# Kernel tuning notes

Measured on AMD Instinct MI355X. Metric: run time of the kernel, lower is better.

## Reference

```python
import jax, jax.numpy as jnp
import numpy as np

D = 768

def _linear_params(key, name_idx, d_in, d_out):
    k1, k2 = jax.random.split(jax.random.fold_in(jax.random.key(42), name_idx))
    bound = 1.0 / np.sqrt(d_in)
    W = jax.random.uniform(k1, (d_out, d_in), jnp.float32, -bound, bound)
    b = jax.random.uniform(k2, (d_out,), jnp.float32, -bound, bound)
    return W, b

def setup_inputs() -> dict:
    key = jax.random.key(0)
    kq, kk, kv = jax.random.split(key, 3)
    B, S = 8, 2048
    inp = {
        'query': jax.random.normal(kq, (B, S, D), jnp.float32),
        'key': jax.random.normal(kk, (B, S, D), jnp.float32),
        'value': jax.random.normal(kv, (B, S, D), jnp.float32),
    }
    Wq, bq = _linear_params(key, 0, D, D)
    Wk, bk = _linear_params(key, 1, D, D)
    Wv, bv = _linear_params(key, 2, D, D)
    Wg1, bg1 = _linear_params(key, 3, D, D)
    Wg2, bg2 = _linear_params(key, 4, D, D)
    inp.update(Wq=Wq, bq=bq, Wk=Wk, bk=bk, Wv=Wv, bv=bv,
               Wg1=Wg1, bg1=bg1, Wg2=Wg2, bg2=bg2,
               text_scale=jnp.ones((1, D), jnp.float32))
    return inp

def reference(query, key, value, Wq, bq, Wk, bk, Wv, bv, Wg1, bg1, Wg2, bg2, text_scale):
    # Linear projections (torch Linear: x @ W.T + b)
    q = jnp.einsum('bsd,ed->bse', query, Wq) + bq
    k = jnp.einsum('bsd,ed->bse', key, Wk) + bk
    v = jnp.einsum('bsd,ed->bse', value, Wv) + bv
    scale = 1.0 / jnp.sqrt(jnp.float32(k.shape[-1]))
    scores = jnp.einsum('bqd,bkd->bqk', q, k) * scale  # [B, S, S]
    attn = jax.nn.softmax(scores, axis=-1)
    attended = jnp.einsum('bqk,bkd->bqd', attn, v)  # dropout = identity (eval)
    # text_gate: Linear -> ReLU -> Linear -> Sigmoid, then sigmoid applied AGAIN (faithful)
    h = jax.nn.relu(jnp.einsum('bsd,ed->bse', attended, Wg1) + bg1)
    gate = jax.nn.sigmoid(jnp.einsum('bsd,ed->bse', h, Wg2) + bg2)
    gated = jax.nn.sigmoid(gate) * attended * text_scale
    return gated
```

## Files before the change

### kernel.cpp

```cpp
#include <hip/hip_runtime.h>

typedef unsigned short ushort_t;
typedef __bf16 bf16x8 __attribute__((ext_vector_type(8)));
typedef float f32x4 __attribute__((ext_vector_type(4)));
typedef short short8 __attribute__((ext_vector_type(8)));

__device__ __forceinline__ float bf2f(unsigned short u) {
    union { unsigned int i; float f; } v; v.i = ((unsigned int)u) << 16; return v.f;
}
__device__ __forceinline__ unsigned short f2bf(float f) {
    union { float f; unsigned int i; } v; v.f = f;
    unsigned int r = v.i + 0x7fffu + ((v.i >> 16) & 1u);
    return (unsigned short)(r >> 16);
}
__device__ __forceinline__ float sigm(float x) { return 1.0f / (1.0f + __expf(-x)); }

__device__ __forceinline__ void async_copy16(const ushort_t* src, ushort_t* dst_lds) {
    __builtin_amdgcn_global_load_lds(
        (const __attribute__((address_space(1))) void*)src,
        (__attribute__((address_space(3))) void*)dst_lds,
        16, 0, 0);
}

#define WSEG 589824
#define NWALL 2949120
#define NTOT 2953728
__global__ __launch_bounds__(256)
void convert_params(const float* __restrict__ Wq, const float* __restrict__ Wk,
                    const float* __restrict__ Wv, const float* __restrict__ Wg1,
                    const float* __restrict__ Wg2, const float* __restrict__ bq,
                    const float* __restrict__ bk, const float* __restrict__ bv,
                    const float* __restrict__ bg1, const float* __restrict__ bg2,
                    const float* __restrict__ ts, ushort_t* __restrict__ dst)
{
    int i = (blockIdx.x * 256 + threadIdx.x) * 8;
    if (i >= NTOT) return;
    const float* src; int off;
    if (i < NWALL) {
        int wi = i / WSEG; off = i - wi * WSEG;
        src = (wi == 0) ? Wq : (wi == 1) ? Wk : (wi == 2) ? Wv : (wi == 3) ? Wg1 : Wg2;
    } else {
        int j = i - NWALL; int bi = j / 768; off = j - bi * 768;
        src = (bi == 0) ? bq : (bi == 1) ? bk : (bi == 2) ? bv : (bi == 3) ? bg1 : (bi == 4) ? bg2 : ts;
    }
    float4 a = *(const float4*)(src + off);
    float4 b = *(const float4*)(src + off + 4);
    short8 o;
    o[0] = (short)f2bf(a.x); o[1] = (short)f2bf(a.y); o[2] = (short)f2bf(a.z); o[3] = (short)f2bf(a.w);
    o[4] = (short)f2bf(b.x); o[5] = (short)f2bf(b.y); o[6] = (short)f2bf(b.z); o[7] = (short)f2bf(b.w);
    *(short8*)(dst + i) = o;
}

template<int EPI, int AF32, int CF32>
__global__ __launch_bounds__(256, 2)
void gemm_bt(const void* __restrict__ Av, const ushort_t* __restrict__ B,
             void* __restrict__ Cv, const ushort_t* __restrict__ bias,
             const ushort_t* __restrict__ aux, const ushort_t* __restrict__ ts,
             int M, int N, int K, float scale,
             long long batchA, long long batchB, long long batchC)
{
    __shared__ __align__(16) ushort_t As[128 * 32];
    __shared__ __align__(16) ushort_t Bs[128 * 32];
    const int tid  = threadIdx.x;
    const int lane = tid & 63;
    const int wave = tid >> 6;
    const int wr = wave >> 1, wc = wave & 1;

    const int gx = gridDim.x, gy = gridDim.y;
    const int nwg = gx * gy * gridDim.z;
    int fid = (blockIdx.z * gy + blockIdx.y) * gx + blockIdx.x;
    fid = (fid & 7) * (nwg >> 3) + (fid >> 3);
    const int bz  = fid / (gx * gy);
    const int rem = fid - bz * (gx * gy);
    const int by  = rem / gx;
    const int bx  = rem - by * gx;
    const int row0 = by * 128;
    const int col0 = bx * 128;

    f32x4 acc[4][4] = {};

    const int srow = tid >> 2;
    const int scol = (tid & 3) * 8;
    const ushort_t* ga0 = (const ushort_t*)Av + batchA * bz + (size_t)(row0 + srow) * K + scol;
    const ushort_t* gb0 = B + batchB * bz + (size_t)(col0 + srow) * K + scol;
    const int arow_s = tid >> 1;
    const int acol_s = (tid & 1) * 16;
    const float* gaf = (const float*)Av + batchA * bz + (size_t)(row0 + arow_s) * K + acol_s;

    const int kop  = (lane >> 4) * 8;
    const int arow = wr * 64 + (lane & 15);
    const int brow = wc * 64 + (lane & 15);

    for (int k0 = 0; k0 < K; k0 += 32) {
        if (AF32) {
            float4 fa0 = *(const float4*)(gaf + k0);
            float4 fa1 = *(const float4*)(gaf + k0 + 4);
            float4 fa2 = *(const float4*)(gaf + k0 + 8);
            float4 fa3 = *(const float4*)(gaf + k0 + 12);
            async_copy16(gb0 + k0,                  Bs + tid * 8);
            async_copy16(gb0 + (size_t)64 * K + k0, Bs + 2048 + tid * 8);
            short8 p0, p1;
            p0[0] = (short)f2bf(fa0.x); p0[1] = (short)f2bf(fa0.y);
            p0[2] = (short)f2bf(fa0.z); p0[3] = (short)f2bf(fa0.w);
            p0[4] = (short)f2bf(fa1.x); p0[5] = (short)f2bf(fa1.y);
            p0[6] = (short)f2bf(fa1.z); p0[7] = (short)f2bf(fa1.w);
            p1[0] = (short)f2bf(fa2.x); p1[1] = (short)f2bf(fa2.y);
            p1[2] = (short)f2bf(fa2.z); p1[3] = (short)f2bf(fa2.w);
            p1[4] = (short)f2bf(fa3.x); p1[5] = (short)f2bf(fa3.y);
            p1[6] = (short)f2bf(fa3.z); p1[7] = (short)f2bf(fa3.w);
            *(short8*)(As + arow_s * 32 + acol_s)     = p0;
            *(short8*)(As + arow_s * 32 + acol_s + 8) = p1;
        } else {
            async_copy16(ga0 + k0,                  As + tid * 8);
            async_copy16(ga0 + (size_t)64 * K + k0, As + 2048 + tid * 8);
            async_copy16(gb0 + k0,                  Bs + tid * 8);
            async_copy16(gb0 + (size_t)64 * K + k0, Bs + 2048 + tid * 8);
        }
        asm volatile("s_waitcnt vmcnt(0)" ::: "memory");
        __syncthreads();

        bf16x8 af[4], bfr[4];
        #pragma unroll
        for (int m = 0; m < 4; ++m)
            af[m] = *(const bf16x8*)(As + (arow + m * 16) * 32 + kop);
        #pragma unroll
        for (int n = 0; n < 4; ++n)
            bfr[n] = *(const bf16x8*)(Bs + (brow + n * 16) * 32 + kop);
        #pragma unroll
        for (int m = 0; m < 4; ++m)
            #pragma unroll
            for (int n = 0; n < 4; ++n)
                acc[m][n] = __builtin_amdgcn_mfma_f32_16x16x32_bf16(af[m], bfr[n], acc[m][n], 0, 0, 0);
        __syncthreads();
    }

    const int r0 = row0 + wr * 64 + (lane >> 4) * 4;
    const int c0 = col0 + wc * 64 + (lane & 15);
    #pragma unroll
    for (int m = 0; m < 4; ++m) {
        #pragma unroll
        for (int n = 0; n < 4; ++n) {
            const int col = c0 + n * 16;
            #pragma unroll
            for (int r = 0; r < 4; ++r) {
                const int row = r0 + m * 16 + r;
                float val = acc[m][n][r];
                if (EPI == 1) {
                    val += bf2f(bias[col]);
                } else if (EPI == 2) {
                    val *= scale;
                } else if (EPI == 3) {
                    val += bf2f(bias[col]);
                    val = fmaxf(val, 0.0f);
                } else if (EPI == 4) {
                    val += bf2f(bias[col]);
                    float g  = sigm(val);
                    float gg = sigm(g);
                    val = gg * bf2f(aux[(size_t)row * N + col]) * bf2f(ts[col]);
                }
                if (CF32) ((float*)Cv)[batchC * bz + (size_t)row * N + col] = val;
                else      ((ushort_t*)Cv)[batchC * bz + (size_t)row * N + col] = f2bf(val);
            }
        }
    }
}

__global__ __launch_bounds__(256)
void softmax_inplace(ushort_t* __restrict__ P, int S)
{
    const size_t row = blockIdx.x;
    ushort_t* p = P + row * (size_t)S;
    const int tid = threadIdx.x;
    const int lane = tid & 63, wave = tid >> 6;

    short8 raw = *(const short8*)(p + tid * 8);
    float x[8];
    #pragma unroll
    for (int j = 0; j < 8; ++j) x[j] = bf2f((unsigned short)raw[j]);

    float mx = x[0];
    #pragma unroll
    for (int j = 1; j < 8; ++j) mx = fmaxf(mx, x[j]);
    #pragma unroll
    for (int o = 32; o > 0; o >>= 1) mx = fmaxf(mx, __shfl_xor(mx, o));
    __shared__ float redm[4], reds[4];
    if (lane == 0) redm[wave] = mx;
    __syncthreads();
    mx = fmaxf(fmaxf(redm[0], redm[1]), fmaxf(redm[2], redm[3]));

    float s = 0.f;
    #pragma unroll
    for (int j = 0; j < 8; ++j) { x[j] = __expf(x[j] - mx); s += x[j]; }
    #pragma unroll
    for (int o = 32; o > 0; o >>= 1) s += __shfl_xor(s, o);
    if (lane == 0) reds[wave] = s;
    __syncthreads();
    s = reds[0] + reds[1] + reds[2] + reds[3];
    const float inv = 1.0f / s;

    short8 outv;
    #pragma unroll
    for (int j = 0; j < 8; ++j) outv[j] = (short)f2bf(x[j] * inv);
    *(short8*)(p + tid * 8) = outv;
}

__global__ __launch_bounds__(256)
void transpose2d(const ushort_t* __restrict__ V, ushort_t* __restrict__ VT, int R, int Ccols)
{
    __shared__ ushort_t t[32][33];
    const size_t zoff = (size_t)blockIdx.z * R * Ccols;
    const int tx = threadIdx.x, ty = threadIdx.y;
    const int c = blockIdx.x * 32 + tx;
    const int rbase = blockIdx.y * 32;
    #pragma unroll
    for (int i = 0; i < 4; ++i)
        t[ty + i * 8][tx] = V[zoff + (size_t)(rbase + ty + i * 8) * Ccols + c];
    __syncthreads();
    const int r = rbase + tx;
    const int cbase = blockIdx.x * 32;
    #pragma unroll
    for (int i = 0; i < 4; ++i)
        VT[zoff + (size_t)(cbase + ty + i * 8) * R + r] = t[tx][ty + i * 8];
}

extern "C" void kernel_launch(void* const* d_in, const int* in_sizes, int n_in,
                              void* d_out, int out_size, void* d_ws, size_t ws_size,
                              hipStream_t stream)
{
    (void)in_sizes; (void)n_in; (void)out_size;
    const float* query = (const float*)d_in[0];
    const float* key_  = (const float*)d_in[1];
    const float* value = (const float*)d_in[2];
    const float* Wq  = (const float*)d_in[3];
    const float* bq  = (const float*)d_in[4];
    const float* Wk  = (const float*)d_in[5];
    const float* bk  = (const float*)d_in[6];
    const float* Wv  = (const float*)d_in[7];
    const float* bv  = (const float*)d_in[8];
    const float* Wg1 = (const float*)d_in[9];
    const float* bg1 = (const float*)d_in[10];
    const float* Wg2 = (const float*)d_in[11];
    const float* bg2 = (const float*)d_in[12];
    const float* tsc = (const float*)d_in[13];

    const int S = 2048, D = 768, Bc = 8;
    const int MS = Bc * S;
    const long long SD = (long long)S * D;
    const long long SS = (long long)S * S;

    char* ws = (char*)d_ws;
    ushort_t* q   = (ushort_t*)(ws);
    ushort_t* att = q;
    ushort_t* k   = (ushort_t*)(ws + 25165824ll);
    ushort_t* h   = k;
    ushort_t* vT  = (ushort_t*)(ws + 50331648ll);
    ushort_t* Wb  = (ushort_t*)(ws + 75497472ll);
    ushort_t* P   = (ushort_t*)(ws + 81404928ll);
    ushort_t* v   = (ushort_t*)d_out;

    const int WQ = 0, WK = 589824, WV = 1179648, WG1 = 1769472, WG2 = 2359296;
    const int BQ = 2949120, BK = 2949888, BV = 2950656, BG1 = 2951424, BG2 = 2952192, TSO = 2952960;

    const dim3 blk(256);
    const float scale = 0.03608439182435161f;
    const bool batched = ws_size >= 148513792ull;

    convert_params<<<dim3((NTOT / 8 + 255) / 256), blk, 0, stream>>>(
        Wq, Wk, Wv, Wg1, Wg2, bq, bk, bv, bg1, bg2, tsc, Wb);
    gemm_bt<1, 1, 0><<<dim3(D / 128, MS / 128), blk, 0, stream>>>(query, Wb + WQ, q, Wb + BQ, nullptr, nullptr, MS, D, D, 1.f, 0, 0, 0);
    gemm_bt<1, 1, 0><<<dim3(D / 128, MS / 128), blk, 0, stream>>>(key_,  Wb + WK, k, Wb + BK, nullptr, nullptr, MS, D, D, 1.f, 0, 0, 0);
    gemm_bt<1, 1, 0><<<dim3(D / 128, MS / 128), blk, 0, stream>>>(value, Wb + WV, v, Wb + BV, nullptr, nullptr, MS, D, D, 1.f, 0, 0, 0);
    transpose2d<<<dim3(D / 32, S / 32, Bc), dim3(32, 8), 0, stream>>>(v, vT, S, D);
    if (batched) {
        gemm_bt<2, 0, 0><<<dim3(S / 128, S / 128, Bc), blk, 0, stream>>>(q, k, P, nullptr, nullptr, nullptr, S, S, D, scale, SD, SD, SS);
        softmax_inplace<<<dim3(MS), blk, 0, stream>>>(P, S);
        gemm_bt<0, 0, 0><<<dim3(D / 128, S / 128, Bc), blk, 0, stream>>>(P, vT, att, nullptr, nullptr, nullptr, S, D, S, 1.f, SS, SD, SD);
    } else {
        for (int z = 0; z < Bc; ++z) {
            gemm_bt<2, 0, 0><<<dim3(S / 128, S / 128), blk, 0, stream>>>(q + (size_t)z * SD, k + (size_t)z * SD, P,
                                                                          nullptr, nullptr, nullptr, S, S, D, scale, 0, 0, 0);
            softmax_inplace<<<dim3(S), blk, 0, stream>>>(P, S);
            gemm_bt<0, 0, 0><<<dim3(D / 128, S / 128), blk, 0, stream>>>(P, vT + (size_t)z * SD, att + (size_t)z * SD,
                                                                          nullptr, nullptr, nullptr, S, D, S, 1.f, 0, 0, 0);
        }
    }
    gemm_bt<3, 0, 0><<<dim3(D / 128, MS / 128), blk, 0, stream>>>(att, Wb + WG1, h, Wb + BG1, nullptr, nullptr, MS, D, D, 1.f, 0, 0, 0);
    gemm_bt<4, 0, 1><<<dim3(D / 128, MS / 128), blk, 0, stream>>>(h, Wb + WG2, d_out, Wb + BG2, att, Wb + TSO, MS, D, D, 1.f, 0, 0, 0);
}
```

Baseline: 374.7 us.

## Replace 128-tile GEMMs with pipelined 256x256 swizzled-LDS GEMM and batch QKV projections

Replaces the simple single-buffered 128x128 GEMM with a 512-thread 256x256-tile kernel. The new kernel double-buffers 64-wide K chunks in XOR-swizzled LDS, interleaves async global-to-LDS copies with MFMA groups under explicit barriers, and raises priority around MFMAs. The fp32 inputs are pre-converted to bf16 in a separate pass so the three QKV projections run as one z-batched launch. The non-batched fallback path is dropped, and the code now always assumes a large workspace. This trades an extra conversion pass and more LDS and registers for higher data reuse and compute/load overlap.

Result: slower. 385.8 us (+3.0%).

```diff
diff --git a/kernel.cpp b/kernel.cpp
--- a/kernel.cpp
+++ b/kernel.cpp
@@ -4,6 +4,9 @@
 typedef __bf16 bf16x8 __attribute__((ext_vector_type(8)));
 typedef float f32x4 __attribute__((ext_vector_type(4)));
 typedef short short8 __attribute__((ext_vector_type(8)));
+
+#define SBAR()   __builtin_amdgcn_s_barrier()
+#define WAITV4() asm volatile("s_waitcnt vmcnt(4)" ::: "memory")
 
 __device__ __forceinline__ float bf2f(unsigned short u) {
     union { unsigned int i; float f; } v; v.i = ((unsigned int)u) << 16; return v.f;
@@ -20,6 +23,10 @@
         (const __attribute__((address_space(1))) void*)src,
         (__attribute__((address_space(3))) void*)dst_lds,
         16, 0, 0);
+}
+
+__device__ __forceinline__ f32x4 MFMA(bf16x8 a, bf16x8 b, f32x4 c) {
+    return __builtin_amdgcn_mfma_f32_16x16x32_bf16(a, b, c, 0, 0, 0);
 }
 
 #define WSEG 589824
@@ -51,20 +58,77 @@
     *(short8*)(dst + i) = o;
 }
 
-template<int EPI, int AF32, int CF32>
-__global__ __launch_bounds__(256, 2)
-void gemm_bt(const void* __restrict__ Av, const ushort_t* __restrict__ B,
-             void* __restrict__ Cv, const ushort_t* __restrict__ bias,
+#define PERT 12582912ll
+__global__ __launch_bounds__(256)
+void convert_inputs(const float* __restrict__ q, const float* __restrict__ k,
+                    const float* __restrict__ v, ushort_t* __restrict__ X)
+{
+    long long i = ((long long)blockIdx.x * 256 + threadIdx.x) * 8;
+    const float* src; long long off;
+    if (i < PERT)          { src = q; off = i; }
+    else if (i < 2 * PERT) { src = k; off = i - PERT; }
+    else                   { src = v; off = i - 2 * PERT; }
+    float4 a = *(const float4*)(src + off);
+    float4 b = *(const float4*)(src + off + 4);
+    short8 o;
+    o[0] = (short)f2bf(a.x); o[1] = (short)f2bf(a.y); o[2] = (short)f2bf(a.z); o[3] = (short)f2bf(a.w);
+    o[4] = (short)f2bf(b.x); o[5] = (short)f2bf(b.y); o[6] = (short)f2bf(b.z); o[7] = (short)f2bf(b.w);
+    *(short8*)(X + i) = o;
+}
+
+template<int NOFF>
+__device__ __forceinline__ void load_b2(bf16x8 (&bF)[4][2], const ushort_t* Bh, int rbase,
+                                        int l15, int k4, int l7)
+{
+    #pragma unroll
+    for (int n = 0; n < 2; ++n) {
+        const int row = rbase + (NOFF + n) * 16 + l15;
+        bF[NOFF + n][0] = *(const bf16x8*)(Bh + (row << 6) + (((0 + k4) ^ l7) << 3));
+        bF[NOFF + n][1] = *(const bf16x8*)(Bh + (row << 6) + (((4 + k4) ^ l7) << 3));
+    }
+}
+__device__ __forceinline__ void load_a4(bf16x8 (&aF)[4][2], const ushort_t* Ah, int moff,
+                                        int l15, int k4, int l7)
+{
+    #pragma unroll
+    for (int m = 0; m < 4; ++m) {
+        const int row = (moff + m) * 16 + l15;
+        aF[m][0] = *(const bf16x8*)(Ah + (row << 6) + (((0 + k4) ^ l7) << 3));
+        aF[m][1] = *(const bf16x8*)(Ah + (row << 6) + (((4 + k4) ^ l7) << 3));
+    }
+}
+template<int MB, int NB>
+__device__ __forceinline__ void mfma16(f32x4 (&acc)[8][4], const bf16x8 (&aF)[4][2],
+                                       const bf16x8 (&bF)[4][2])
+{
+    __builtin_amdgcn_s_setprio(1);
+    #pragma unroll
+    for (int m = 0; m < 4; ++m)
+        #pragma unroll
+        for (int n = 0; n < 2; ++n) {
+            acc[MB + m][NB + n] = MFMA(aF[m][0], bF[NB + n][0], acc[MB + m][NB + n]);
+            acc[MB + m][NB + n] = MFMA(aF[m][1], bF[NB + n][1], acc[MB + m][NB + n]);
+        }
+    __builtin_amdgcn_s_setprio(0);
+}
+
+template<int EPI, int CF32>
+__global__ __launch_bounds__(512, 1)
+void gemm256(const ushort_t* __restrict__ A, const ushort_t* __restrict__ B,
+             void* __restrict__ Cv, void* __restrict__ Cv2,
+             const ushort_t* __restrict__ bias,
              const ushort_t* __restrict__ aux, const ushort_t* __restrict__ ts,
              int M, int N, int K, float scale,
              long long batchA, long long batchB, long long batchC)
 {
-    __shared__ __align__(16) ushort_t As[128 * 32];
-    __shared__ __align__(16) ushort_t Bs[128 * 32];
+    __shared__ __align__(16) ushort_t As[2][2][8192];
+    __shared__ __align__(16) ushort_t Bs[2][2][8192];
     const int tid  = threadIdx.x;
     const int lane = tid & 63;
-    const int wave = tid >> 6;
-    const int wr = wave >> 1, wc = wave & 1;
+    const int wid  = tid >> 6;
+    const int wr = wid >> 2;
+    const int wc = wid & 3;
+    const int l15 = lane & 15, k4 = lane >> 4, l7 = lane & 7;
 
     const int gx = gridDim.x, gy = gridDim.y;
     const int nwg = gx * gy * gridDim.z;
@@ -74,70 +138,104 @@
     const int rem = fid - bz * (gx * gy);
     const int by  = rem / gx;
     const int bx  = rem - by * gx;
-    const int row0 = by * 128;
-    const int col0 = bx * 128;
-
-    f32x4 acc[4][4] = {};
-
-    const int srow = tid >> 2;
-    const int scol = (tid & 3) * 8;
-    const ushort_t* ga0 = (const ushort_t*)Av + batchA * bz + (size_t)(row0 + srow) * K + scol;
-    const ushort_t* gb0 = B + batchB * bz + (size_t)(col0 + srow) * K + scol;
-    const int arow_s = tid >> 1;
-    const int acol_s = (tid & 1) * 16;
-    const float* gaf = (const float*)Av + batchA * bz + (size_t)(row0 + arow_s) * K + acol_s;
-
-    const int kop  = (lane >> 4) * 8;
-    const int arow = wr * 64 + (lane & 15);
-    const int brow = wc * 64 + (lane & 15);
-
-    for (int k0 = 0; k0 < K; k0 += 32) {
-        if (AF32) {
-            float4 fa0 = *(const float4*)(gaf + k0);
-            float4 fa1 = *(const float4*)(gaf + k0 + 4);
-            float4 fa2 = *(const float4*)(gaf + k0 + 8);
-            float4 fa3 = *(const float4*)(gaf + k0 + 12);
-            async_copy16(gb0 + k0,                  Bs + tid * 8);
-            async_copy16(gb0 + (size_t)64 * K + k0, Bs + 2048 + tid * 8);
-            short8 p0, p1;
-            p0[0] = (short)f2bf(fa0.x); p0[1] = (short)f2bf(fa0.y);
-            p0[2] = (short)f2bf(fa0.z); p0[3] = (short)f2bf(fa0.w);
-            p0[4] = (short)f2bf(fa1.x); p0[5] = (short)f2bf(fa1.y);
-            p0[6] = (short)f2bf(fa1.z); p0[7] = (short)f2bf(fa1.w);
-            p1[0] = (short)f2bf(fa2.x); p1[1] = (short)f2bf(fa2.y);
-            p1[2] = (short)f2bf(fa2.z); p1[3] = (short)f2bf(fa2.w);
-            p1[4] = (short)f2bf(fa3.x); p1[5] = (short)f2bf(fa3.y);
-            p1[6] = (short)f2bf(fa3.z); p1[7] = (short)f2bf(fa3.w);
-            *(short8*)(As + arow_s * 32 + acol_s)     = p0;
-            *(short8*)(As + arow_s * 32 + acol_s + 8) = p1;
-        } else {
-            async_copy16(ga0 + k0,                  As + tid * 8);
-            async_copy16(ga0 + (size_t)64 * K + k0, As + 2048 + tid * 8);
-            async_copy16(gb0 + k0,                  Bs + tid * 8);
-            async_copy16(gb0 + (size_t)64 * K + k0, Bs + 2048 + tid * 8);
-        }
-        asm volatile("s_waitcnt vmcnt(0)" ::: "memory");
-        __syncthreads();
-
-        bf16x8 af[4], bfr[4];
-        #pragma unroll
-        for (int m = 0; m < 4; ++m)
-            af[m] = *(const bf16x8*)(As + (arow + m * 16) * 32 + kop);
-        #pragma unroll
-        for (int n = 0; n < 4; ++n)
-            bfr[n] = *(const bf16x8*)(Bs + (brow + n * 16) * 32 + kop);
-        #pragma unroll
-        for (int m = 0; m < 4; ++m)
-            #pragma unroll
-            for (int n = 0; n < 4; ++n)
-                acc[m][n] = __builtin_amdgcn_mfma_f32_16x16x32_bf16(af[m], bfr[n], acc[m][n], 0, 0, 0);
-        __syncthreads();
-    }
-
-    const int r0 = row0 + wr * 64 + (lane >> 4) * 4;
-    const int c0 = col0 + wc * 64 + (lane & 15);
-    #pragma unroll
-    for (int m = 0; m < 4; ++m) {
+    const int row0 = by * 256;
+    const int col0 = bx * 256;
+
+    const ushort_t* Ab = A + batchA * bz;
+    const ushort_t* Bb = B + batchB * bz;
+
+    const int srow  = tid >> 3;
+    const int sslot = (tid & 7) ^ (srow & 7);
+    const ushort_t* aB0 = Ab + (size_t)(row0 + srow) * K + sslot * 8;
+    const ushort_t* aB1 = aB0 + (size_t)128 * K;
+    const ushort_t* bB0 = Bb + (size_t)(col0 + srow) * K + sslot * 8;
+    const ushort_t* bB1 = bB0 + (size_t)128 * K;
+
+    ushort_t* A00 = &As[0][0][0]; ushort_t* A01 = &As[0][1][0];
+    ushort_t* A10 = &As[1][0][0]; ushort_t* A11 = &As[1][1][0];
+    ushort_t* B00 = &Bs[0][0][0]; ushort_t* B01 = &Bs[0][1][0];
+    ushort_t* B10 = &Bs[1][0][0]; ushort_t* B11 = &Bs[1][1][0];
+
+#define STAGE(G, L) do { \
+    async_copy16((G), (L) + tid * 8); \
+    async_copy16((G) + (size_t)64 * K, (L) + 4096 + tid * 8); \
+} while (0)
+
+    const ushort_t* Ah0 = &As[0][wr][0];
+    const ushort_t* Ah1 = &As[1][wr][0];
+    const ushort_t* Bh0 = &Bs[0][wc >> 1][0];
+    const ushort_t* Bh1 = &Bs[1][wc >> 1][0];
+    const int brbase = (wc & 1) * 64;
+
+    f32x4 acc[8][4] = {};
+    bf16x8 aF[4][2], bF[4][2];
+
+    const int NT  = K >> 6;
+    const int NT2 = NT >> 1;
+
+    STAGE(bB0, B00); STAGE(bB1, B01);
+    STAGE(aB0, A00); STAGE(aB1, A01);
+    STAGE(bB0 + 64, B10); STAGE(bB1 + 64, B11);
+    WAITV4();
+    SBAR();
+
+    for (int i = 0; i < NT2; ++i) {
+        const int t1 = 2 * i + 1;
+        int t2 = 2 * i + 2; if (t2 >= NT) t2 -= NT;
+        int t3 = 2 * i + 3; if (t3 >= NT) t3 -= NT;
+        load_a4(aF, Ah0, 0, l15, k4, l7);
+        load_b2<0>(bF, Bh0, brbase, l15, k4, l7);
+        STAGE(aB0 + (size_t)t1 * 64, A10);
+        SBAR();
+        mfma16<0, 0>(acc, aF, bF);
+        SBAR();
+        load_b2<2>(bF, Bh0, brbase, l15, k4, l7);
+        STAGE(aB1 + (size_t)t1 * 64, A11);
+        SBAR();
+        mfma16<0, 2>(acc, aF, bF);
+        SBAR();
+        load_a4(aF, Ah0, 4, l15, k4, l7);
+        STAGE(bB0 + (size_t)t2 * 64, B00);
+        SBAR();
+        mfma16<4, 0>(acc, aF, bF);
+        SBAR();
+        STAGE(bB1 + (size_t)t2 * 64, B01);
+        WAITV4();
+        SBAR();
+        mfma16<4, 2>(acc, aF, bF);
+        SBAR();
+        load_a4(aF, Ah1, 0, l15, k4, l7);
+        load_b2<0>(bF, Bh1, brbase, l15, k4, l7);
+        STAGE(aB0 + (size_t)t2 * 64, A00);
+        SBAR();
+        mfma16<0, 0>(acc, aF, bF);
+        SBAR();
+        load_b2<2>(bF, Bh1, brbase, l15, k4, l7);
+        STAGE(aB1 + (size_t)t2 * 64, A01);
+        SBAR();
+        mfma16<0, 2>(acc, aF, bF);
+        SBAR();
+        load_a4(aF, Ah1, 4, l15, k4, l7);
+        STAGE(bB0 + (size_t)t3 * 64, B10);
+        SBAR();
+        mfma16<4, 0>(acc, aF, bF);
+        SBAR();
+        STAGE(bB1 + (size_t)t3 * 64, B11);
+        WAITV4();
+        SBAR();
+        mfma16<4, 2>(acc, aF, bF);
+        SBAR();
+    }
+#undef STAGE
+
+    ushort_t* Cb = (EPI == 1 &&  true)
+                   ? ((bz == 2) ? (ushort_t*)Cv2 : (ushort_t*)Cv + batchC * bz)
+                   : (ushort_t*)Cv + (CF32 ? 0 : batchC * bz);
+    float* Cf = (float*)Cv;
+    const int r0 = row0 + wr * 128 + (lane >> 4) * 4;
+    const int c0 = col0 + wc * 64 + l15;
+    #pragma unroll
+    for (int m = 0; m < 8; ++m) {
         #pragma unroll
         for (int n = 0; n < 4; ++n) {
             const int col = c0 + n * 16;
@@ -146,7 +244,7 @@
                 const int row = r0 + m * 16 + r;
                 float val = acc[m][n][r];
                 if (EPI == 1) {
-                    val += bf2f(bias[col]);
+                    val += bf2f(bias[bz * 768 + col]);
                 } else if (EPI == 2) {
                     val *= scale;
                 } else if (EPI == 3) {
@@ -158,8 +256,8 @@
                     float gg = sigm(g);
                     val = gg * bf2f(aux[(size_t)row * N + col]) * bf2f(ts[col]);
                 }
-                if (CF32) ((float*)Cv)[batchC * bz + (size_t)row * N + col] = val;
-                else      ((ushort_t*)Cv)[batchC * bz + (size_t)row * N + col] = f2bf(val);
+                if (CF32) Cf[(size_t)row * N + col] = val;
+                else      Cb[(size_t)row * N + col] = f2bf(val);
             }
         }
     }
@@ -227,7 +325,7 @@
                               void* d_out, int out_size, void* d_ws, size_t ws_size,
                               hipStream_t stream)
 {
-    (void)in_sizes; (void)n_in; (void)out_size;
+    (void)in_sizes; (void)n_in; (void)out_size; (void)ws_size;
     const float* query = (const float*)d_in[0];
     const float* key_  = (const float*)d_in[1];
     const float* value = (const float*)d_in[2];
@@ -247,6 +345,7 @@
     const int MS = Bc * S;
     const long long SD = (long long)S * D;
     const long long SS = (long long)S * S;
+    const long long MSD = (long long)MS * D;
 
     char* ws = (char*)d_ws;
     ushort_t* q   = (ushort_t*)(ws);
@@ -254,36 +353,30 @@
     ushort_t* k   = (ushort_t*)(ws + 25165824ll);
     ushort_t* h   = k;
     ushort_t* vT  = (ushort_t*)(ws + 50331648ll);
-    ushort_t* Wb  = (ushort_t*)(ws + 75497472ll);
-    ushort_t* P   = (ushort_t*)(ws + 81404928ll);
+    ushort_t* X   = (ushort_t*)(ws + 50331648ll);
+    ushort_t* P   = (ushort_t*)(ws + 75497472ll);
+    ushort_t* Wb  = (ushort_t*)(ws + 142606336ll);
     ushort_t* v   = (ushort_t*)d_out;
 
-    const int WQ = 0, WK = 589824, WV = 1179648, WG1 = 1769472, WG2 = 2359296;
-    const int BQ = 2949120, BK = 2949888, BV = 2950656, BG1 = 2951424, BG2 = 2952192, TSO = 2952960;
-
-    const dim3 blk(256);
+    const int WQ = 0, WG1 = 1769472, WG2 = 2359296;
+    const int BQ = 2949120, BG1 = 2951424, BG2 = 2952192, TSO = 2952960;
+
+    const dim3 blk(256), blk5(512);
     const float scale = 0.03608439182435161f;
-    const bool batched = ws_size >= 148513792ull;
 
     convert_params<<<dim3((NTOT / 8 + 255) / 256), blk, 0, stream>>>(
         Wq, Wk, Wv, Wg1, Wg2, bq, bk, bv, bg1, bg2, tsc, Wb);
-    gemm_bt<1, 1, 0><<<dim3(D / 128, MS / 128), blk, 0, stream>>>(query, Wb + WQ, q, Wb + BQ, nullptr, nullptr, MS, D, D, 1.f, 0, 0, 0);
-    gemm_bt<1, 1, 0><<<dim3(D / 128, MS / 128), blk, 0, stream>>>(key_,  Wb + WK, k, Wb + BK, nullptr, nullptr, MS, D, D, 1.f, 0, 0, 0);
-    gemm_bt<1, 1, 0><<<dim3(D / 128, MS / 128), blk, 0, stream>>>(value, Wb + WV, v, Wb + BV, nullptr, nullptr, MS, D, D, 1.f, 0, 0, 0);
+    convert_inputs<<<dim3(18432), blk, 0, stream>>>(query, key_, value, X);
+    gemm256<1, 0><<<dim3(D / 256, MS / 256, 3), blk5, 0, stream>>>(
+        X, Wb + WQ, q, v, Wb + BQ, nullptr, nullptr, MS, D, D, 1.f, MSD, (long long)WSEG, MSD);
     transpose2d<<<dim3(D / 32, S / 32, Bc), dim3(32, 8), 0, stream>>>(v, vT, S, D);
-    if (batched) {
-        gemm_bt<2, 0, 0><<<dim3(S / 128, S / 128, Bc), blk, 0, stream>>>(q, k, P, nullptr, nullptr, nullptr, S, S, D, scale, SD, SD, SS);
-        softmax_inplace<<<dim3(MS), blk, 0, stream>>>(P, S);
-        gemm_bt<0, 0, 0><<<dim3(D / 128, S / 128, Bc), blk, 0, stream>>>(P, vT, att, nullptr, nullptr, nullptr, S, D, S, 1.f, SS, SD, SD);
-    } else {
-        for (int z = 0; z < Bc; ++z) {
-            gemm_bt<2, 0, 0><<<dim3(S / 128, S / 128), blk, 0, stream>>>(q + (size_t)z * SD, k + (size_t)z * SD, P,
-                                                                          nullptr, nullptr, nullptr, S, S, D, scale, 0, 0, 0);
-            softmax_inplace<<<dim3(S), blk, 0, stream>>>(P, S);
-            gemm_bt<0, 0, 0><<<dim3(D / 128, S / 128), blk, 0, stream>>>(P, vT + (size_t)z * SD, att + (size_t)z * SD,
-                                                                          nullptr, nullptr, nullptr, S, D, S, 1.f, 0, 0, 0);
-        }
-    }
-    gemm_bt<3, 0, 0><<<dim3(D / 128, MS / 128), blk, 0, stream>>>(att, Wb + WG1, h, Wb + BG1, nullptr, nullptr, MS, D, D, 1.f, 0, 0, 0);
-    gemm_bt<4, 0, 1><<<dim3(D / 128, MS / 128), blk, 0, stream>>>(h, Wb + WG2, d_out, Wb + BG2, att, Wb + TSO, MS, D, D, 1.f, 0, 0, 0);
-}
+    gemm256<2, 0><<<dim3(S / 256, S / 256, Bc), blk5, 0, stream>>>(
+        q, k, P, nullptr, nullptr, nullptr, nullptr, S, S, D, scale, SD, SD, SS);
+    softmax_inplace<<<dim3(MS), blk, 0, stream>>>(P, S);
+    gemm256<0, 0><<<dim3(D / 256, S / 256, Bc), blk5, 0, stream>>>(
+        P, vT, att, nullptr, nullptr, nullptr, nullptr, S, D, S, 1.f, SS, SD, SD);
+    gemm256<3, 0><<<dim3(D / 256, MS / 256, 1), blk5, 0, stream>>>(
+        att, Wb + WG1, h, nullptr, Wb + BG1, nullptr, nullptr, MS, D, D, 1.f, 0, 0, 0);
+    gemm256<4, 1><<<dim3(D / 256, MS / 256, 1), blk5, 0, stream>>>(
+        h, Wb + WG2, d_out, nullptr, Wb + BG2, att, Wb + TSO, MS, D, D, 1.f, 0, 0, 0);
+}
```
